# Optimization experiments

Measured on AMD Instinct MI355X. Metric: run time of the kernel, lower is better.

The kernel has to match this reference:

```python
import jax, jax.numpy as jnp
import numpy as np

# Dimensions per init_kwargs / input_specs
B, N, C = 8192, 4, 2048          # tokens, expansion_rate, hidden_dim
SINKHORN_ITERS = 20
EPS = 1e-5
ALPHA_INIT = 0.01


def setup_inputs() -> dict:
    key = jax.random.key(0)
    k1, k2 = jax.random.split(key)
    return {
        "x_expanded": jax.random.normal(k1, (B, N, C), dtype=jnp.float32),
        "rmsnorm_weight": jnp.ones((C,), dtype=jnp.float32),   # init: ones
        "H_pre": jnp.zeros((N,), dtype=jnp.float32),            # init: zeros
        "H_post": jnp.zeros((N,), dtype=jnp.float32),           # init: zeros
        "H_res": ALPHA_INIT * jax.random.normal(k2, (N, N), dtype=jnp.float32),
    }


def _sinkhorn(M, iters, eps):
    """Iterative row/column normalization -> (approximately) doubly-stochastic."""
    def body(_, M):
        M = M / (jnp.sum(M, axis=1, keepdims=True) + eps)  # row normalize
        M = M / (jnp.sum(M, axis=0, keepdims=True) + eps)  # col normalize
        return M
    return jax.lax.fori_loop(0, iters, body, M)


def reference(x_expanded, rmsnorm_weight, H_pre, H_post, H_res):
    # RMSNorm over hidden dim C, per (token, branch)
    ms = jnp.mean(x_expanded * x_expanded, axis=-1, keepdims=True)  # [B, N, 1]
    x_norm = x_expanded * jax.lax.rsqrt(ms + EPS) * rmsnorm_weight  # [B, N, C]

    # Manifold-constrained residual mixing matrix (doubly stochastic via Sinkhorn)
    H = _sinkhorn(jnp.exp(H_res), SINKHORN_ITERS, EPS)              # [N, N]

    pre = jax.nn.sigmoid(H_pre)    # [N] input-aggregation weights
    post = jax.nn.sigmoid(H_post)  # [N] output-distribution weights

    # Aggregate normalized branches into a single stream, redistribute,
    # and add the Sinkhorn-mixed residual of the raw branches.
    x_agg = jnp.einsum('n,bnc->bc', pre, x_norm)                     # [B, C]
    y = jnp.einsum('mn,bnc->bmc', H, x_expanded) \
        + post[None, :, None] * x_agg[:, None, :]                    # [B, N, C]
    return y
```

## Files before the change

### kernel.cpp

```cpp
#include <hip/hip_runtime.h>
#include <math.h>

#define B_TOK 8192
#define NB 4
#define CH 2048
#define TPB 256
#define SINK_ITERS 20
#define EPS 1e-5f

__global__ void mhc_sinkhorn(const float* __restrict__ H_pre,
                             const float* __restrict__ H_post,
                             const float* __restrict__ H_res,
                             float* __restrict__ ws)
{
    if (threadIdx.x == 0) {
        float M[NB][NB];
        #pragma unroll
        for (int i = 0; i < NB; ++i)
            #pragma unroll
            for (int j = 0; j < NB; ++j)
                M[i][j] = expf(H_res[i * NB + j]);

        for (int it = 0; it < SINK_ITERS; ++it) {
            #pragma unroll
            for (int i = 0; i < NB; ++i) {
                float s = M[i][0] + M[i][1] + M[i][2] + M[i][3] + EPS;
                float r = 1.0f / s;
                #pragma unroll
                for (int j = 0; j < NB; ++j) M[i][j] *= r;
            }
            #pragma unroll
            for (int j = 0; j < NB; ++j) {
                float s = M[0][j] + M[1][j] + M[2][j] + M[3][j] + EPS;
                float r = 1.0f / s;
                #pragma unroll
                for (int i = 0; i < NB; ++i) M[i][j] *= r;
            }
        }
        #pragma unroll
        for (int i = 0; i < NB; ++i)
            #pragma unroll
            for (int j = 0; j < NB; ++j)
                ws[i * NB + j] = M[i][j];
        #pragma unroll
        for (int n = 0; n < NB; ++n) {
            ws[16 + n] = 1.0f / (1.0f + expf(-H_pre[n]));
            ws[20 + n] = 1.0f / (1.0f + expf(-H_post[n]));
        }
    }
}

__global__ __launch_bounds__(TPB) void mhc_main(const float* __restrict__ x,
                                                const float* __restrict__ w,
                                                const float* __restrict__ ws,
                                                float* __restrict__ y)
{
    const int b = blockIdx.x;
    const int t = threadIdx.x;
    const int wave = t >> 6;
    const int lane = t & 63;

    float H[NB][NB], pre[NB], post[NB];
    #pragma unroll
    for (int i = 0; i < NB; ++i)
        #pragma unroll
        for (int j = 0; j < NB; ++j)
            H[i][j] = ws[i * NB + j];
    #pragma unroll
    for (int n = 0; n < NB; ++n) {
        pre[n]  = ws[16 + n];
        post[n] = ws[20 + n];
    }

    const float4* xb = (const float4*)(x + (size_t)b * NB * CH);
    float4 xv[NB][2];
    float ss[NB];
    #pragma unroll
    for (int n = 0; n < NB; ++n) {
        xv[n][0] = xb[n * (CH / 4) + t];
        xv[n][1] = xb[n * (CH / 4) + (TPB) + t];
        float4 a = xv[n][0], c = xv[n][1];
        ss[n] = a.x * a.x + a.y * a.y + a.z * a.z + a.w * a.w +
                c.x * c.x + c.y * c.y + c.z * c.z + c.w * c.w;
    }

    #pragma unroll
    for (int m = 1; m < 64; m <<= 1) {
        #pragma unroll
        for (int n = 0; n < NB; ++n)
            ss[n] += __shfl_xor(ss[n], m);
    }
    __shared__ float red[4][NB];
    if (lane == 0) {
        #pragma unroll
        for (int n = 0; n < NB; ++n) red[wave][n] = ss[n];
    }
    __syncthreads();

    float inv[NB];
    #pragma unroll
    for (int n = 0; n < NB; ++n) {
        float tot = red[0][n] + red[1][n] + red[2][n] + red[3][n];
        inv[n] = rsqrtf(tot * (1.0f / CH) + EPS);
    }

    const float4* wv4 = (const float4*)w;
    float4 w0 = wv4[t], w1 = wv4[TPB + t];
    float wv[8] = { w0.x, w0.y, w0.z, w0.w, w1.x, w1.y, w1.z, w1.w };

    float xr[NB][8];
    #pragma unroll
    for (int n = 0; n < NB; ++n) {
        xr[n][0] = xv[n][0].x; xr[n][1] = xv[n][0].y;
        xr[n][2] = xv[n][0].z; xr[n][3] = xv[n][0].w;
        xr[n][4] = xv[n][1].x; xr[n][5] = xv[n][1].y;
        xr[n][6] = xv[n][1].z; xr[n][7] = xv[n][1].w;
    }

    float agg[8];
    #pragma unroll
    for (int k = 0; k < 8; ++k) {
        float a = 0.0f;
        #pragma unroll
        for (int n = 0; n < NB; ++n)
            a += pre[n] * (xr[n][k] * inv[n] * wv[k]);
        agg[k] = a;
    }

    float4* yb = (float4*)(y + (size_t)b * NB * CH);
    #pragma unroll
    for (int m = 0; m < NB; ++m) {
        float out[8];
        #pragma unroll
        for (int k = 0; k < 8; ++k) {
            float v = post[m] * agg[k];
            #pragma unroll
            for (int n = 0; n < NB; ++n)
                v += H[m][n] * xr[n][k];
            out[k] = v;
        }
        float4 o0 = { out[0], out[1], out[2], out[3] };
        float4 o1 = { out[4], out[5], out[6], out[7] };
        yb[m * (CH / 4) + t]       = o0;
        yb[m * (CH / 4) + TPB + t] = o1;
    }
}

extern "C" void kernel_launch(void* const* d_in, const int* in_sizes, int n_in,
                              void* d_out, int out_size, void* d_ws, size_t ws_size,
                              hipStream_t stream) {
    const float* x      = (const float*)d_in[0];
    const float* wgt    = (const float*)d_in[1];
    const float* h_pre  = (const float*)d_in[2];
    const float* h_post = (const float*)d_in[3];
    const float* h_res  = (const float*)d_in[4];
    float* y  = (float*)d_out;
    float* ws = (float*)d_ws;

    mhc_sinkhorn<<<1, 64, 0, stream>>>(h_pre, h_post, h_res, ws);
    mhc_main<<<B_TOK, TPB, 0, stream>>>(x, wgt, ws, y);
}
```

Baseline: 112.4 us.

## Fuse Sinkhorn into main kernel and process four tokens per block

Drops the separate single-thread Sinkhorn kernel and its workspace round trip. Every thread now recomputes the 4x4 Sinkhorn normalization and the sigmoid gates, then broadcasts them with readfirstlane. Each block also handles four tokens in sequence instead of one, so this setup cost and the weight load are spread over several tokens. In exchange there is redundant per-thread scalar work, an extra barrier per token, and fewer blocks in flight for hiding memory latency in what is a bandwidth-bound kernel.

```diff
diff --git a/kernel.cpp b/kernel.cpp
--- a/kernel.cpp
+++ b/kernel.cpp
@@ -5,144 +5,138 @@
 #define NB 4
 #define CH 2048
 #define TPB 256
+#define TOK_PER_BLK 4
+#define NBLK (B_TOK / TOK_PER_BLK)
 #define SINK_ITERS 20
 #define EPS 1e-5f
 
-__global__ void mhc_sinkhorn(const float* __restrict__ H_pre,
-                             const float* __restrict__ H_post,
-                             const float* __restrict__ H_res,
-                             float* __restrict__ ws)
-{
-    if (threadIdx.x == 0) {
-        float M[NB][NB];
-        #pragma unroll
-        for (int i = 0; i < NB; ++i)
-            #pragma unroll
-            for (int j = 0; j < NB; ++j)
-                M[i][j] = expf(H_res[i * NB + j]);
-
-        for (int it = 0; it < SINK_ITERS; ++it) {
-            #pragma unroll
-            for (int i = 0; i < NB; ++i) {
-                float s = M[i][0] + M[i][1] + M[i][2] + M[i][3] + EPS;
-                float r = 1.0f / s;
-                #pragma unroll
-                for (int j = 0; j < NB; ++j) M[i][j] *= r;
-            }
-            #pragma unroll
-            for (int j = 0; j < NB; ++j) {
-                float s = M[0][j] + M[1][j] + M[2][j] + M[3][j] + EPS;
-                float r = 1.0f / s;
-                #pragma unroll
-                for (int i = 0; i < NB; ++i) M[i][j] *= r;
-            }
-        }
-        #pragma unroll
-        for (int i = 0; i < NB; ++i)
-            #pragma unroll
-            for (int j = 0; j < NB; ++j)
-                ws[i * NB + j] = M[i][j];
-        #pragma unroll
-        for (int n = 0; n < NB; ++n) {
-            ws[16 + n] = 1.0f / (1.0f + expf(-H_pre[n]));
-            ws[20 + n] = 1.0f / (1.0f + expf(-H_post[n]));
-        }
-    }
+__device__ __forceinline__ float bcast_first(float v) {
+    return __uint_as_float(__builtin_amdgcn_readfirstlane(__float_as_uint(v)));
 }
 
-__global__ __launch_bounds__(TPB) void mhc_main(const float* __restrict__ x,
-                                                const float* __restrict__ w,
-                                                const float* __restrict__ ws,
-                                                float* __restrict__ y)
+__global__ __launch_bounds__(TPB) void mhc_fused(
+    const float* __restrict__ x,
+    const float* __restrict__ w,
+    const float* __restrict__ H_pre,
+    const float* __restrict__ H_post,
+    const float* __restrict__ H_res,
+    float* __restrict__ y)
 {
-    const int b = blockIdx.x;
     const int t = threadIdx.x;
     const int wave = t >> 6;
     const int lane = t & 63;
+
+    const float4* wv4 = (const float4*)w;
+    float4 w0 = wv4[t], w1 = wv4[TPB + t];
+
+    float M[NB][NB];
+    #pragma unroll
+    for (int i = 0; i < NB; ++i)
+        #pragma unroll
+        for (int j = 0; j < NB; ++j)
+            M[i][j] = expf(H_res[i * NB + j]);
+
+    for (int s = 0; s < SINK_ITERS; ++s) {
+        #pragma unroll
+        for (int i = 0; i < NB; ++i) {
+            float r = 1.0f / (M[i][0] + M[i][1] + M[i][2] + M[i][3] + EPS);
+            #pragma unroll
+            for (int j = 0; j < NB; ++j) M[i][j] *= r;
+        }
+        #pragma unroll
+        for (int j = 0; j < NB; ++j) {
+            float r = 1.0f / (M[0][j] + M[1][j] + M[2][j] + M[3][j] + EPS);
+            #pragma unroll
+            for (int i = 0; i < NB; ++i) M[i][j] *= r;
+        }
+    }
 
     float H[NB][NB], pre[NB], post[NB];
     #pragma unroll
     for (int i = 0; i < NB; ++i)
         #pragma unroll
         for (int j = 0; j < NB; ++j)
-            H[i][j] = ws[i * NB + j];
+            H[i][j] = bcast_first(M[i][j]);
     #pragma unroll
     for (int n = 0; n < NB; ++n) {
-        pre[n]  = ws[16 + n];
-        post[n] = ws[20 + n];
+        pre[n]  = bcast_first(1.0f / (1.0f + expf(-H_pre[n])));
+        post[n] = bcast_first(1.0f / (1.0f + expf(-H_post[n])));
     }
 
-    const float4* xb = (const float4*)(x + (size_t)b * NB * CH);
-    float4 xv[NB][2];
-    float ss[NB];
-    #pragma unroll
-    for (int n = 0; n < NB; ++n) {
-        xv[n][0] = xb[n * (CH / 4) + t];
-        xv[n][1] = xb[n * (CH / 4) + (TPB) + t];
-        float4 a = xv[n][0], c = xv[n][1];
-        ss[n] = a.x * a.x + a.y * a.y + a.z * a.z + a.w * a.w +
-                c.x * c.x + c.y * c.y + c.z * c.z + c.w * c.w;
-    }
+    __shared__ float red[4][NB];
 
-    #pragma unroll
-    for (int m = 1; m < 64; m <<= 1) {
+    for (int it = 0; it < TOK_PER_BLK; ++it) {
+        const int b = blockIdx.x * TOK_PER_BLK + it;
+
+        const float4* xb = (const float4*)(x + (size_t)b * NB * CH);
+        float4 xv[NB][2];
+        float ss[NB];
         #pragma unroll
-        for (int n = 0; n < NB; ++n)
-            ss[n] += __shfl_xor(ss[n], m);
-    }
-    __shared__ float red[4][NB];
-    if (lane == 0) {
+        for (int n = 0; n < NB; ++n) {
+            xv[n][0] = xb[n * (CH / 4) + t];
+            xv[n][1] = xb[n * (CH / 4) + TPB + t];
+            float4 a = xv[n][0], c = xv[n][1];
+            ss[n] = a.x * a.x + a.y * a.y + a.z * a.z + a.w * a.w +
+                    c.x * c.x + c.y * c.y + c.z * c.z + c.w * c.w;
+        }
+
         #pragma unroll
-        for (int n = 0; n < NB; ++n) red[wave][n] = ss[n];
-    }
-    __syncthreads();
+        for (int m = 1; m < 64; m <<= 1) {
+            #pragma unroll
+            for (int n = 0; n < NB; ++n)
+                ss[n] += __shfl_xor(ss[n], m);
+        }
+        if (lane == 0) {
+            #pragma unroll
+            for (int n = 0; n < NB; ++n) red[wave][n] = ss[n];
+        }
+        __syncthreads();
 
-    float inv[NB];
-    #pragma unroll
-    for (int n = 0; n < NB; ++n) {
-        float tot = red[0][n] + red[1][n] + red[2][n] + red[3][n];
-        inv[n] = rsqrtf(tot * (1.0f / CH) + EPS);
-    }
+        float inv[NB];
+        #pragma unroll
+        for (int n = 0; n < NB; ++n) {
+            float tot = red[0][n] + red[1][n] + red[2][n] + red[3][n];
+            inv[n] = rsqrtf(tot * (1.0f / CH) + EPS);
+        }
+        __syncthreads();
 
-    const float4* wv4 = (const float4*)w;
-    float4 w0 = wv4[t], w1 = wv4[TPB + t];
-    float wv[8] = { w0.x, w0.y, w0.z, w0.w, w1.x, w1.y, w1.z, w1.w };
+        float xr[NB][8];
+        #pragma unroll
+        for (int n = 0; n < NB; ++n) {
+            xr[n][0] = xv[n][0].x; xr[n][1] = xv[n][0].y;
+            xr[n][2] = xv[n][0].z; xr[n][3] = xv[n][0].w;
+            xr[n][4] = xv[n][1].x; xr[n][5] = xv[n][1].y;
+            xr[n][6] = xv[n][1].z; xr[n][7] = xv[n][1].w;
+        }
+        float wv[8] = { w0.x, w0.y, w0.z, w0.w, w1.x, w1.y, w1.z, w1.w };
 
-    float xr[NB][8];
-    #pragma unroll
-    for (int n = 0; n < NB; ++n) {
-        xr[n][0] = xv[n][0].x; xr[n][1] = xv[n][0].y;
-        xr[n][2] = xv[n][0].z; xr[n][3] = xv[n][0].w;
-        xr[n][4] = xv[n][1].x; xr[n][5] = xv[n][1].y;
-        xr[n][6] = xv[n][1].z; xr[n][7] = xv[n][1].w;
-    }
-
-    float agg[8];
-    #pragma unroll
-    for (int k = 0; k < 8; ++k) {
-        float a = 0.0f;
-        #pragma unroll
-        for (int n = 0; n < NB; ++n)
-            a += pre[n] * (xr[n][k] * inv[n] * wv[k]);
-        agg[k] = a;
-    }
-
-    float4* yb = (float4*)(y + (size_t)b * NB * CH);
-    #pragma unroll
-    for (int m = 0; m < NB; ++m) {
-        float out[8];
+        float agg[8];
         #pragma unroll
         for (int k = 0; k < 8; ++k) {
-            float v = post[m] * agg[k];
+            float a = 0.0f;
             #pragma unroll
             for (int n = 0; n < NB; ++n)
-                v += H[m][n] * xr[n][k];
-            out[k] = v;
+                a += pre[n] * (xr[n][k] * inv[n] * wv[k]);
+            agg[k] = a;
         }
-        float4 o0 = { out[0], out[1], out[2], out[3] };
-        float4 o1 = { out[4], out[5], out[6], out[7] };
-        yb[m * (CH / 4) + t]       = o0;
-        yb[m * (CH / 4) + TPB + t] = o1;
+
+        float4* yb = (float4*)(y + (size_t)b * NB * CH);
+        #pragma unroll
+        for (int m = 0; m < NB; ++m) {
+            float out[8];
+            #pragma unroll
+            for (int k = 0; k < 8; ++k) {
+                float v = post[m] * agg[k];
+                #pragma unroll
+                for (int n = 0; n < NB; ++n)
+                    v += H[m][n] * xr[n][k];
+                out[k] = v;
+            }
+            float4 o0 = { out[0], out[1], out[2], out[3] };
+            float4 o1 = { out[4], out[5], out[6], out[7] };
+            yb[m * (CH / 4) + t]       = o0;
+            yb[m * (CH / 4) + TPB + t] = o1;
+        }
     }
 }
 
@@ -154,9 +148,7 @@
     const float* h_pre  = (const float*)d_in[2];
     const float* h_post = (const float*)d_in[3];
     const float* h_res  = (const float*)d_in[4];
-    float* y  = (float*)d_out;
-    float* ws = (float*)d_ws;
+    float* y = (float*)d_out;
 
-    mhc_sinkhorn<<<1, 64, 0, stream>>>(h_pre, h_post, h_res, ws);
-    mhc_main<<<B_TOK, TPB, 0, stream>>>(x, wgt, ws, y);
+    mhc_fused<<<NBLK, TPB, 0, stream>>>(x, wgt, h_pre, h_post, h_res, y);
 }
```

Result: slower. 118.0 us (+4.9%).
